# Kernel optimization log

Hardware: AMD Instinct MI355X
Metric: run time of the kernel (lower is better)

The kernel has to match this reference:

```python
import jax, jax.numpy as jnp
import numpy as np
import itertools

B, N, C, O = 16, 32, 8, 16
IN_DIMS = [C + 2 * C, C + C + 2 * C, (C + C + 2 * C) * 2, (C + C) * 6]  # [24, 32, 64, 96]


def _expand(x, n):
    # Expander: broadcast order-k tensor [..., C] to order-(k+1) [..., n, C]
    return jnp.broadcast_to(x[..., None, :], x.shape[:-1] + (n, x.shape[-1]))


def _reduce(x, exclude_self=True):
    # Reducer: max ('exists') and min ('forall') over the last object axis,
    # optionally excluding the diagonal of the last two object axes.
    n = x.shape[-2]
    if exclude_self and x.ndim >= 4:  # batch + >=2 object axes + channel
        m = (1.0 - jnp.eye(n, dtype=x.dtype))[:, :, None]  # [N, N, 1]
        x_max = (x * m).max(axis=-2)
        x_min = (x * m + (1.0 - m)).min(axis=-2)
    else:
        x_max = x.max(axis=-2)
        x_min = x.min(axis=-2)
    return jnp.concatenate([x_max, x_min], axis=-1)


def _permute(x, order):
    # Permutation: concat all order! permutations of the object axes on channels.
    if order <= 1:
        return x
    perms = itertools.permutations(range(1, order + 1))
    return jnp.concatenate([jnp.transpose(x, (0,) + p + (order + 1,)) for p in perms], axis=-1)


def _logic(f, W, b):
    # DLMInferenceBase stand-in: per-group inference MLP with sigmoid output.
    return jax.nn.sigmoid(f @ W + b)


def setup_inputs() -> dict:
    key = jax.random.key(0)
    ks = jax.random.split(key, 12)
    inp = {
        'x0': jax.random.uniform(ks[0], (B, C), dtype=jnp.float32),
        'x1': jax.random.uniform(ks[1], (B, N, C), dtype=jnp.float32),
        'x2': jax.random.uniform(ks[2], (B, N, N, C), dtype=jnp.float32),
        'x3': jax.random.uniform(ks[3], (B, N, N, N, C), dtype=jnp.float32),
    }
    for i, d in enumerate(IN_DIMS):
        inp[f'W{i}'] = jax.random.normal(ks[4 + i], (d, O), dtype=jnp.float32) * 0.05
        inp[f'b{i}'] = jnp.zeros((O,), dtype=jnp.float32)
    return inp


def reference(x0, x1, x2, x3, W0, b0, W1, b1, W2, b2, W3, b3):
    n = x1.shape[1]
    # order 0: input + reduce(order1)           -> [B, 24]
    f0 = jnp.concatenate([x0, _reduce(x1)], axis=-1)
    # order 1: expand(order0) + input + reduce(order2) -> [B, N, 32]
    f1 = jnp.concatenate([_expand(x0, n), x1, _reduce(x2)], axis=-1)
    # order 2: (expand + input + reduce) x 2 perms -> [B, N, N, 64]
    f2 = _permute(jnp.concatenate([_expand(x1, n), x2, _reduce(x3)], axis=-1), 2)
    # order 3: (expand + input) x 6 perms -> [B, N, N, N, 96]
    f3 = _permute(jnp.concatenate([_expand(x2, n), x3], axis=-1), 3)
    return (_logic(f0, W0, b0), _logic(f1, W1, b1), _logic(f2, W2, b2), _logic(f3, W3, b3))
```

## Files before the change

kernel.cpp:

```cpp
#include <hip/hip_runtime.h>
#include <hip/hip_bf16.h>

#define FP const float* __restrict__

__device__ __forceinline__ void load8(const float* p, float* o) {
    const float4* v = reinterpret_cast<const float4*>(p);
    float4 a = v[0], b = v[1];
    o[0] = a.x; o[1] = a.y; o[2] = a.z; o[3] = a.w;
    o[4] = b.x; o[5] = b.y; o[6] = b.z; o[7] = b.w;
}

__device__ __forceinline__ float sigmoidf_(float x) {
    return 1.0f / (1.0f + __expf(-x));
}

__device__ __forceinline__ void store16_f32(float* p, const float* y) {
    float4* d = reinterpret_cast<float4*>(p);
    d[0] = make_float4(y[0], y[1], y[2], y[3]);
    d[1] = make_float4(y[4], y[5], y[6], y[7]);
    d[2] = make_float4(y[8], y[9], y[10], y[11]);
    d[3] = make_float4(y[12], y[13], y[14], y[15]);
}

__device__ __forceinline__ void fma_block2(const float s[2][8], const float* Wrow,
                                           float acc[2][16]) {
#pragma unroll
    for (int c = 0; c < 8; ++c) {
        const float4* wv = reinterpret_cast<const float4*>(Wrow + c * 16);
#pragma unroll
        for (int o4 = 0; o4 < 4; ++o4) {
            float4 wq = wv[o4];
#pragma unroll
            for (int r = 0; r < 2; ++r) {
                acc[r][o4 * 4 + 0] += s[r][c] * wq.x;
                acc[r][o4 * 4 + 1] += s[r][c] * wq.y;
                acc[r][o4 * 4 + 2] += s[r][c] * wq.z;
                acc[r][o4 * 4 + 3] += s[r][c] * wq.w;
            }
        }
    }
}

__global__ __launch_bounds__(256) void k_fused(
    FP x0, FP x1, FP x2, FP x3, FP W0, FP b0, FP W1, FP b1, FP W2, FP b2, FP W3, FP b3,
    float* __restrict__ out0, float* __restrict__ out1, float* __restrict__ out2,
    float* __restrict__ out3) {
    __shared__ float sm[3072];
    const int blk = blockIdx.x;
    const int tid = threadIdx.x;

    if (blk < 1024) {
        float* Ws = sm;
        float* bs = sm + 1536;
        for (int t = tid; t < 1536; t += 256) Ws[t] = W3[t];
        if (tid < 16) bs[tid] = b3[tid];
        __syncthreads();
        int xcd = blk & 7, inner = blk >> 3;
        int r64 = inner & 63, hb = inner >> 6;
        int lb = xcd | (hb << 3);
        int t3 = (lb * 64 + r64) * 256 + tid;
        int w0 = (t3 & 15) * 2;
        int v = (t3 >> 4) & 31;
        int u = (t3 >> 9) & 31;
        int b = t3 >> 14;
        const size_t bu = (size_t)(b * 32 + u);
        const size_t bv = (size_t)(b * 32 + v);
        const size_t bb = (size_t)(b * 32);

        float x2uv[8], x2vu[8];
        load8(x2 + (bu * 32 + v) * 8, x2uv);
        load8(x2 + (bv * 32 + u) * 8, x2vu);
        float acc[2][16];
        {
            float base[16];
#pragma unroll
            for (int o = 0; o < 16; ++o) base[o] = bs[o];
#pragma unroll
            for (int c = 0; c < 8; ++c) {
                const float4* wa = reinterpret_cast<const float4*>(Ws + (0 + c) * 16);
                const float4* wb = reinterpret_cast<const float4*>(Ws + (32 + c) * 16);
#pragma unroll
                for (int o4 = 0; o4 < 4; ++o4) {
                    float4 qa = wa[o4], qb = wb[o4];
                    base[o4 * 4 + 0] += x2uv[c] * qa.x + x2vu[c] * qb.x;
                    base[o4 * 4 + 1] += x2uv[c] * qa.y + x2vu[c] * qb.y;
                    base[o4 * 4 + 2] += x2uv[c] * qa.z + x2vu[c] * qb.z;
                    base[o4 * 4 + 3] += x2uv[c] * qa.w + x2vu[c] * qb.w;
                }
            }
#pragma unroll
            for (int r = 0; r < 2; ++r)
#pragma unroll
                for (int o = 0; o < 16; ++o) acc[r][o] = base[o];
        }

        float s[2][8];
#pragma unroll
        for (int r = 0; r < 2; ++r) load8(x2 + (bu * 32 + (w0 + r)) * 8, s[r]);
        fma_block2(s, Ws + 16 * 16, acc);
#pragma unroll
        for (int r = 0; r < 2; ++r) load8(x2 + ((bb + (w0 + r)) * 32 + u) * 8, s[r]);
        fma_block2(s, Ws + 48 * 16, acc);
#pragma unroll
        for (int r = 0; r < 2; ++r) load8(x2 + (bv * 32 + (w0 + r)) * 8, s[r]);
        fma_block2(s, Ws + 64 * 16, acc);
#pragma unroll
        for (int r = 0; r < 2; ++r) load8(x2 + ((bb + (w0 + r)) * 32 + v) * 8, s[r]);
        fma_block2(s, Ws + 80 * 16, acc);
#pragma unroll
        for (int r = 0; r < 2; ++r) load8(x3 + ((bu * 32 + v) * 32 + (w0 + r)) * 8, s[r]);
        fma_block2(s, Ws + 8 * 16, acc);
#pragma unroll
        for (int r = 0; r < 2; ++r) load8(x3 + ((bu * 32 + (w0 + r)) * 32 + v) * 8, s[r]);
        fma_block2(s, Ws + 24 * 16, acc);
#pragma unroll
        for (int r = 0; r < 2; ++r) load8(x3 + ((bv * 32 + u) * 32 + (w0 + r)) * 8, s[r]);
        fma_block2(s, Ws + 40 * 16, acc);
#pragma unroll
        for (int r = 0; r < 2; ++r) load8(x3 + (((bb + (w0 + r)) * 32 + u) * 32 + v) * 8, s[r]);
        fma_block2(s, Ws + 56 * 16, acc);
#pragma unroll
        for (int r = 0; r < 2; ++r) load8(x3 + ((bv * 32 + (w0 + r)) * 32 + u) * 8, s[r]);
        fma_block2(s, Ws + 72 * 16, acc);
#pragma unroll
        for (int r = 0; r < 2; ++r) load8(x3 + (((bb + (w0 + r)) * 32 + v) * 32 + u) * 8, s[r]);
        fma_block2(s, Ws + 88 * 16, acc);

        size_t row0 = ((bu * 32 + v) * 32 + w0);
#pragma unroll
        for (int r = 0; r < 2; ++r) {
            float y[16];
#pragma unroll
            for (int o = 0; o < 16; ++o) y[o] = sigmoidf_(acc[r][o]);
            store16_f32(out3 + (row0 + r) * 16, y);
        }
    } else if (blk < 1536) {
        float* Ws = sm;
        float* bs = sm + 1024;
        float* sx1 = sm + 1040;
        float* sx2ij = sm + 1296;
        float* sx2ji = sm + 1552;
        float* rAmax = sm + 1808;
        float* rAmin = sm + 2064;
        float* rBmax = sm + 2320;
        float* rBmin = sm + 2576;
        int q = blk - 1024;
        int xcd = q & 7, inner = q >> 3;
        int i = inner & 31;
        int b = xcd | ((inner >> 5) << 3);
        int bi = b * 32 + i;
        int j = tid >> 3, c = tid & 7;
        for (int t = tid; t < 1024; t += 256) Ws[t] = W2[t];
        if (tid < 16) bs[tid] = b2[tid];
        sx1[tid] = x1[(size_t)b * 256 + tid];
        sx2ij[tid] = x2[(size_t)bi * 256 + tid];
        sx2ji[tid] = x2[(((size_t)b * 32 + j) * 32 + i) * 8 + c];
        {
            const float* pA = x3 + ((size_t)bi * 32 + j) * 256 + c;
            const float* pB = x3 + (((size_t)b * 32 + j) * 32 + i) * 256 + c;
            float amax = -1e30f, amin = 1e30f, bmax = -1e30f, bmin = 1e30f;
            for (int w = 0; w < 32; ++w) {
                float va = pA[w * 8], vb = pB[w * 8];
                bool dA = (w == j), dB = (w == i);
                amax = fmaxf(amax, dA ? 0.0f : va);
                amin = fminf(amin, dA ? 1.0f : va);
                bmax = fmaxf(bmax, dB ? 0.0f : vb);
                bmin = fminf(bmin, dB ? 1.0f : vb);
            }
            rAmax[tid] = amax; rAmin[tid] = amin;
            rBmax[tid] = bmax; rBmin[tid] = bmin;
        }
        __syncthreads();
#pragma unroll
        for (int qq = 0; qq < 2; ++qq) {
            int idx = tid + qq * 256;
            int j2 = idx >> 4, o = idx & 15;
            float acc = bs[o];
#pragma unroll
            for (int cc = 0; cc < 8; ++cc) {
                int jc = j2 * 8 + cc;
                acc += sx1[i * 8 + cc] * Ws[(0 + cc) * 16 + o];
                acc += sx2ij[jc] * Ws[(8 + cc) * 16 + o];
                acc += rAmax[jc] * Ws[(16 + cc) * 16 + o];
                acc += rAmin[jc] * Ws[(24 + cc) * 16 + o];
                acc += sx1[jc] * Ws[(32 + cc) * 16 + o];
                acc += sx2ji[jc] * Ws[(40 + cc) * 16 + o];
                acc += rBmax[jc] * Ws[(48 + cc) * 16 + o];
                acc += rBmin[jc] * Ws[(56 + cc) * 16 + o];
            }
            out2[((size_t)bi * 32 + j2) * 16 + o] = sigmoidf_(acc);
        }
    } else {
        float* s2max = sm;
        float* s2min = sm + 256;
        float* sx1 = sm + 512;
        float* sx0 = sm + 768;
        float* m1max = sm + 776;
        float* m1min = sm + 784;
        int b = blk - 1536;
        int i = tid >> 3, c = tid & 7;
        {
            const float* p = x2 + ((size_t)(b * 32 + i) * 32) * 8 + c;
            float vmax = -1e30f, vmin = 1e30f;
            for (int j2 = 0; j2 < 32; ++j2) {
                float v = p[j2 * 8];
                vmax = fmaxf(vmax, (j2 == i) ? 0.0f : v);
                vmin = fminf(vmin, (j2 == i) ? 1.0f : v);
            }
            s2max[tid] = vmax;
            s2min[tid] = vmin;
        }
        sx1[tid] = x1[(size_t)b * 256 + tid];
        if (tid < 8) sx0[tid] = x0[b * 8 + tid];
        __syncthreads();
        if (tid < 8) {
            float mx = -1e30f, mn = 1e30f;
            for (int ii = 0; ii < 32; ++ii) {
                float v = sx1[ii * 8 + tid];
                mx = fmaxf(mx, v);
                mn = fminf(mn, v);
            }
            m1max[tid] = mx;
            m1min[tid] = mn;
        }
        __syncthreads();
#pragma unroll
        for (int qq = 0; qq < 2; ++qq) {
            int idx = tid + qq * 256;
            int i2 = idx >> 4, o = idx & 15;
            float acc = b1[o];
#pragma unroll
            for (int cc = 0; cc < 8; ++cc) {
                acc += sx0[cc] * W1[cc * 16 + o];
                acc += sx1[i2 * 8 + cc] * W1[(8 + cc) * 16 + o];
                acc += s2max[i2 * 8 + cc] * W1[(16 + cc) * 16 + o];
                acc += s2min[i2 * 8 + cc] * W1[(24 + cc) * 16 + o];
            }
            out1[((size_t)b * 32 + i2) * 16 + o] = sigmoidf_(acc);
        }
        if (tid < 16) {
            int o = tid;
            float acc = b0[o];
#pragma unroll
            for (int cc = 0; cc < 8; ++cc) {
                acc += sx0[cc] * W0[cc * 16 + o];
                acc += m1max[cc] * W0[(8 + cc) * 16 + o];
                acc += m1min[cc] * W0[(16 + cc) * 16 + o];
            }
            out0[b * 16 + o] = sigmoidf_(acc);
        }
    }
}

extern "C" void kernel_launch(void* const* d_in, const int* in_sizes, int n_in, void* d_out,
                              int out_size, void* d_ws, size_t ws_size, hipStream_t stream) {
    const float *x0 = nullptr, *x1 = nullptr, *x2 = nullptr, *x3 = nullptr;
    const float *W0 = nullptr, *W1 = nullptr, *W2 = nullptr, *W3 = nullptr;
    const float* bb[4] = {nullptr, nullptr, nullptr, nullptr};
    int nb = 0;
    for (int k = 0; k < n_in; ++k) {
        const float* p = (const float*)d_in[k];
        switch (in_sizes[k]) {
            case 128:     x0 = p; break;
            case 4096:    x1 = p; break;
            case 131072:  x2 = p; break;
            case 4194304: x3 = p; break;
            case 384:     W0 = p; break;
            case 512:     W1 = p; break;
            case 1024:    W2 = p; break;
            case 1536:    W3 = p; break;
            case 16:      if (nb < 4) bb[nb++] = p; break;
            default: break;
        }
    }
    if (!x0) x0 = (const float*)d_in[0];
    if (!x1) x1 = (const float*)d_in[1];
    if (!x2) x2 = (const float*)d_in[2];
    if (!x3) x3 = (const float*)d_in[3];
    if (!W0) W0 = (const float*)d_in[4];
    if (!W1) W1 = (const float*)d_in[6];
    if (!W2) W2 = (const float*)d_in[8];
    if (!W3) W3 = (const float*)d_in[10];
    const float* b0 = nb > 0 ? bb[0] : (const float*)d_in[5];
    const float* b1 = nb > 1 ? bb[1] : (const float*)d_in[7];
    const float* b2 = nb > 2 ? bb[2] : (const float*)d_in[9];
    const float* b3 = nb > 3 ? bb[3] : (const float*)d_in[11];

    float* out = (float*)d_out;
    float* out0 = out;
    float* out1 = out + 256;
    float* out2 = out + 8448;
    float* out3 = out + 270592;

    k_fused<<<1552, 256, 0, stream>>>(x0, x1, x2, x3, W0, b0, W1, b1, W2, b2, W3, b3,
                                      out0, out1, out2, out3);
}
```

Before: 124.2 us.

## Compute order-3 logic layer with bf16 MFMA instead of scalar FP32 FMAs

Replaces the per-thread FP32 FMA loop for the order-3 output with wave-level 16x16x32 bf16 MFMA instructions. Each wave handles 16 output rows, gathers the permuted x2/x3 features into bf16 fragments and loads W3 fragments directly from global memory. The order-3 grid grows from 1024 to 8192 blocks, with each lane writing scalar outputs. Inputs and weights are rounded to bf16, which lowers precision, and the more scattered stores and extra block-scheduling overhead may offset the arithmetic savings.

```diff
diff --git a/kernel.cpp b/kernel.cpp
--- a/kernel.cpp
+++ b/kernel.cpp
@@ -2,6 +2,9 @@
 #include <hip/hip_bf16.h>
 
 #define FP const float* __restrict__
+
+typedef __attribute__((ext_vector_type(8))) short bf16x8;
+typedef __attribute__((ext_vector_type(4))) float f32x4;
 
 __device__ __forceinline__ void load8(const float* p, float* o) {
     const float4* v = reinterpret_cast<const float4*>(p);
@@ -14,31 +17,18 @@
     return 1.0f / (1.0f + __expf(-x));
 }
 
-__device__ __forceinline__ void store16_f32(float* p, const float* y) {
-    float4* d = reinterpret_cast<float4*>(p);
-    d[0] = make_float4(y[0], y[1], y[2], y[3]);
-    d[1] = make_float4(y[4], y[5], y[6], y[7]);
-    d[2] = make_float4(y[8], y[9], y[10], y[11]);
-    d[3] = make_float4(y[12], y[13], y[14], y[15]);
-}
-
-__device__ __forceinline__ void fma_block2(const float s[2][8], const float* Wrow,
-                                           float acc[2][16]) {
-#pragma unroll
-    for (int c = 0; c < 8; ++c) {
-        const float4* wv = reinterpret_cast<const float4*>(Wrow + c * 16);
-#pragma unroll
-        for (int o4 = 0; o4 < 4; ++o4) {
-            float4 wq = wv[o4];
-#pragma unroll
-            for (int r = 0; r < 2; ++r) {
-                acc[r][o4 * 4 + 0] += s[r][c] * wq.x;
-                acc[r][o4 * 4 + 1] += s[r][c] * wq.y;
-                acc[r][o4 * 4 + 2] += s[r][c] * wq.z;
-                acc[r][o4 * 4 + 3] += s[r][c] * wq.w;
-            }
-        }
-    }
+__device__ __forceinline__ short f2bf(float x) {
+    __hip_bfloat16 h = __float2bfloat16(x);
+    return *reinterpret_cast<short*>(&h);
+}
+
+__device__ __forceinline__ bf16x8 load8_bf(const float* p) {
+    float v[8];
+    load8(p, v);
+    bf16x8 r;
+#pragma unroll
+    for (int j = 0; j < 8; ++j) r[j] = f2bf(v[j]);
+    return r;
 }
 
 __global__ __launch_bounds__(256) void k_fused(
@@ -49,92 +39,58 @@
     const int blk = blockIdx.x;
     const int tid = threadIdx.x;
 
-    if (blk < 1024) {
-        float* Ws = sm;
-        float* bs = sm + 1536;
-        for (int t = tid; t < 1536; t += 256) Ws[t] = W3[t];
-        if (tid < 16) bs[tid] = b3[tid];
-        __syncthreads();
-        int xcd = blk & 7, inner = blk >> 3;
-        int r64 = inner & 63, hb = inner >> 6;
-        int lb = xcd | (hb << 3);
-        int t3 = (lb * 64 + r64) * 256 + tid;
-        int w0 = (t3 & 15) * 2;
-        int v = (t3 >> 4) & 31;
-        int u = (t3 >> 9) & 31;
-        int b = t3 >> 14;
-        const size_t bu = (size_t)(b * 32 + u);
-        const size_t bv = (size_t)(b * 32 + v);
-        const size_t bb = (size_t)(b * 32);
-
-        float x2uv[8], x2vu[8];
-        load8(x2 + (bu * 32 + v) * 8, x2uv);
-        load8(x2 + (bv * 32 + u) * 8, x2vu);
-        float acc[2][16];
-        {
-            float base[16];
-#pragma unroll
-            for (int o = 0; o < 16; ++o) base[o] = bs[o];
-#pragma unroll
-            for (int c = 0; c < 8; ++c) {
-                const float4* wa = reinterpret_cast<const float4*>(Ws + (0 + c) * 16);
-                const float4* wb = reinterpret_cast<const float4*>(Ws + (32 + c) * 16);
-#pragma unroll
-                for (int o4 = 0; o4 < 4; ++o4) {
-                    float4 qa = wa[o4], qb = wb[o4];
-                    base[o4 * 4 + 0] += x2uv[c] * qa.x + x2vu[c] * qb.x;
-                    base[o4 * 4 + 1] += x2uv[c] * qa.y + x2vu[c] * qb.y;
-                    base[o4 * 4 + 2] += x2uv[c] * qa.z + x2vu[c] * qb.z;
-                    base[o4 * 4 + 3] += x2uv[c] * qa.w + x2vu[c] * qb.w;
-                }
-            }
-#pragma unroll
-            for (int r = 0; r < 2; ++r)
-#pragma unroll
-                for (int o = 0; o < 16; ++o) acc[r][o] = base[o];
-        }
-
-        float s[2][8];
-#pragma unroll
-        for (int r = 0; r < 2; ++r) load8(x2 + (bu * 32 + (w0 + r)) * 8, s[r]);
-        fma_block2(s, Ws + 16 * 16, acc);
-#pragma unroll
-        for (int r = 0; r < 2; ++r) load8(x2 + ((bb + (w0 + r)) * 32 + u) * 8, s[r]);
-        fma_block2(s, Ws + 48 * 16, acc);
-#pragma unroll
-        for (int r = 0; r < 2; ++r) load8(x2 + (bv * 32 + (w0 + r)) * 8, s[r]);
-        fma_block2(s, Ws + 64 * 16, acc);
-#pragma unroll
-        for (int r = 0; r < 2; ++r) load8(x2 + ((bb + (w0 + r)) * 32 + v) * 8, s[r]);
-        fma_block2(s, Ws + 80 * 16, acc);
-#pragma unroll
-        for (int r = 0; r < 2; ++r) load8(x3 + ((bu * 32 + v) * 32 + (w0 + r)) * 8, s[r]);
-        fma_block2(s, Ws + 8 * 16, acc);
-#pragma unroll
-        for (int r = 0; r < 2; ++r) load8(x3 + ((bu * 32 + (w0 + r)) * 32 + v) * 8, s[r]);
-        fma_block2(s, Ws + 24 * 16, acc);
-#pragma unroll
-        for (int r = 0; r < 2; ++r) load8(x3 + ((bv * 32 + u) * 32 + (w0 + r)) * 8, s[r]);
-        fma_block2(s, Ws + 40 * 16, acc);
-#pragma unroll
-        for (int r = 0; r < 2; ++r) load8(x3 + (((bb + (w0 + r)) * 32 + u) * 32 + v) * 8, s[r]);
-        fma_block2(s, Ws + 56 * 16, acc);
-#pragma unroll
-        for (int r = 0; r < 2; ++r) load8(x3 + ((bv * 32 + (w0 + r)) * 32 + u) * 8, s[r]);
-        fma_block2(s, Ws + 72 * 16, acc);
-#pragma unroll
-        for (int r = 0; r < 2; ++r) load8(x3 + (((bb + (w0 + r)) * 32 + v) * 32 + u) * 8, s[r]);
-        fma_block2(s, Ws + 88 * 16, acc);
-
-        size_t row0 = ((bu * 32 + v) * 32 + w0);
-#pragma unroll
-        for (int r = 0; r < 2; ++r) {
-            float y[16];
-#pragma unroll
-            for (int o = 0; o < 16; ++o) y[o] = sigmoidf_(acc[r][o]);
-            store16_f32(out3 + (row0 + r) * 16, y);
-        }
-    } else if (blk < 1536) {
+    if (blk < 8192) {
+        const int lane = tid & 63;
+        const int wv = tid >> 6;
+        const int q = lane >> 4;
+        const int mn = lane & 15;
+        const int xcd = blk & 7, inner = blk >> 3;
+        const int b = xcd + 8 * (inner >> 9);
+        const int tb = (inner & 511) * 4 + wv;
+        const int u = tb >> 6;
+        const int v = (tb >> 1) & 31;
+        const int w0 = (tb & 1) * 16;
+        const int w = w0 + mn;
+        const unsigned bu = b * 32 + u, bv = b * 32 + v, bbs = b * 32;
+
+        bf16x8 Bf[3];
+#pragma unroll
+        for (int kb = 0; kb < 3; ++kb) {
+#pragma unroll
+            for (int j = 0; j < 8; ++j)
+                Bf[kb][j] = f2bf(W3[(kb * 32 + q * 8 + j) * 16 + mn]);
+        }
+        const float bias = b3[mn];
+        f32x4 acc = {bias, bias, bias, bias};
+
+        {
+            unsigned e2 = (q == 0) ? (bu * 32 + v) : (bu * 32 + w);
+            unsigned e3 = (q == 1) ? ((bu * 32 + v) * 32 + w) : ((bu * 32 + w) * 32 + v);
+            const float* p = (q & 1) ? (x3 + (size_t)e3 * 8) : (x2 + (size_t)e2 * 8);
+            bf16x8 a = load8_bf(p);
+            acc = __builtin_amdgcn_mfma_f32_16x16x32_bf16(a, Bf[0], acc, 0, 0, 0);
+        }
+        {
+            unsigned e2 = (q == 0) ? (bv * 32 + u) : ((bbs + w) * 32 + u);
+            unsigned e3 = (q == 1) ? ((bv * 32 + u) * 32 + w) : (((bbs + w) * 32 + u) * 32 + v);
+            const float* p = (q & 1) ? (x3 + (size_t)e3 * 8) : (x2 + (size_t)e2 * 8);
+            bf16x8 a = load8_bf(p);
+            acc = __builtin_amdgcn_mfma_f32_16x16x32_bf16(a, Bf[1], acc, 0, 0, 0);
+        }
+        {
+            unsigned e2 = (q == 0) ? (bv * 32 + w) : ((bbs + w) * 32 + v);
+            unsigned e3 = (q == 1) ? ((bv * 32 + w) * 32 + u) : (((bbs + w) * 32 + v) * 32 + u);
+            const float* p = (q & 1) ? (x3 + (size_t)e3 * 8) : (x2 + (size_t)e2 * 8);
+            bf16x8 a = load8_bf(p);
+            acc = __builtin_amdgcn_mfma_f32_16x16x32_bf16(a, Bf[2], acc, 0, 0, 0);
+        }
+
+        const size_t rowbase = ((size_t)bu * 32 + v) * 32 + w0;
+#pragma unroll
+        for (int rr = 0; rr < 4; ++rr) {
+            out3[(rowbase + q * 4 + rr) * 16 + mn] = sigmoidf_(acc[rr]);
+        }
+    } else if (blk < 8704) {
         float* Ws = sm;
         float* bs = sm + 1024;
         float* sx1 = sm + 1040;
@@ -144,8 +100,8 @@
         float* rAmin = sm + 2064;
         float* rBmax = sm + 2320;
         float* rBmin = sm + 2576;
-        int q = blk - 1024;
-        int xcd = q & 7, inner = q >> 3;
+        int qq0 = blk - 8192;
+        int xcd = qq0 & 7, inner = qq0 >> 3;
         int i = inner & 31;
         int b = xcd | ((inner >> 5) << 3);
         int bi = b * 32 + i;
@@ -197,7 +153,7 @@
         float* sx0 = sm + 768;
         float* m1max = sm + 776;
         float* m1min = sm + 784;
-        int b = blk - 1536;
+        int b = blk - 8704;
         int i = tid >> 3, c = tid & 7;
         {
             const float* p = x2 + ((size_t)(b * 32 + i) * 32) * 8 + c;
@@ -292,6 +248,6 @@
     float* out2 = out + 8448;
     float* out3 = out + 270592;
 
-    k_fused<<<1552, 256, 0, stream>>>(x0, x1, x2, x3, W0, b0, W1, b1, W2, b2, W3, b3,
+    k_fused<<<8720, 256, 0, stream>>>(x0, x1, x2, x3, W0, b0, W1, b1, W2, b2, W3, b3,
                                       out0, out1, out2, out3);
 }
```

Result: faster. 120.4 us (-3.0%).
